# Kernel optimization log

Hardware: AMD Instinct MI355X
Metric: run time of the kernel (lower is better)

The kernel has to match this reference:

```python
import jax, jax.numpy as jnp
import numpy as np

WINDOW_SYNC = 20   # min(20, T//2) with T=8192
WINDOW_SURGE = 10
BN_EPS = 1e-5      # BatchNorm1d eval-mode, running_mean=0, running_var=1


def _corr_matrix(x):
    # x: [w, A] observations x variables -> [A, A] Pearson correlation
    xc = x - x.mean(0)
    cov = xc.T @ xc
    d = jnp.sqrt(jnp.diag(cov))
    return cov / (d[:, None] * d[None, :])


def _offdiag_mean(C):
    A = C.shape[0]
    return (C.sum() - jnp.trace(C)) / (A * (A - 1))


def _rolling_offdiag_corr(returns, window):
    # mean off-diagonal correlation over each trailing window [i-window, i)
    T, A = returns.shape
    starts = jnp.arange(T - window)
    def one(s):
        w = jax.lax.dynamic_slice(returns, (s, 0), (window, A))
        return _offdiag_mean(_corr_matrix(w))
    return jax.vmap(one)(starts)


def setup_inputs() -> dict:
    key = jax.random.key(0)
    ks = jax.random.split(key, 10)
    T, A, H = 8192, 128, 128
    returns_sequence = jax.random.normal(ks[0], (T, A), dtype=jnp.float32) * 0.02
    positions = jax.random.normal(ks[1], (A,), dtype=jnp.float32)
    s1 = 1.0 / np.sqrt(2 * A)
    s2 = 1.0 / np.sqrt(H)
    s3 = 1.0 / np.sqrt(H // 2)
    return {
        "returns_sequence": returns_sequence,
        "positions": positions,
        "w1": jax.random.uniform(ks[2], (2 * A, H), jnp.float32, -s1, s1),
        "b1": jax.random.uniform(ks[3], (H,), jnp.float32, -s1, s1),
        "gamma": jnp.ones((H,), jnp.float32),
        "beta": jnp.zeros((H,), jnp.float32),
        "w2": jax.random.uniform(ks[4], (H, H // 2), jnp.float32, -s2, s2),
        "b2": jax.random.uniform(ks[5], (H // 2,), jnp.float32, -s2, s2),
        "w3": jax.random.uniform(ks[6], (H // 2, 3), jnp.float32, -s3, s3),
        "b3": jax.random.uniform(ks[7], (3,), jnp.float32, -s3, s3),
    }


def reference(returns_sequence, positions, w1, b1, gamma, beta, w2, b2, w3, b3):
    returns = returns_sequence
    T, A = returns.shape

    # ---- herding index ----
    cs_std = jnp.std(returns, axis=1, ddof=1)                 # [T]
    herding_trend = -jnp.diff(cs_std).mean()
    avg_dispersion = cs_std.mean()
    herding_index = jnp.clip(herding_trend / (avg_dispersion + 1e-6) + 0.5, 0.0, 1.0)

    # ---- synchronization ----
    corr = _corr_matrix(returns)                              # [A, A]
    avg_correlation = _offdiag_mean(corr)
    rolling = _rolling_offdiag_corr(returns, WINDOW_SYNC)     # [T-20]
    phase_locking = (rolling > 0.7).astype(jnp.float32).mean()
    eigvals = jnp.linalg.eigvalsh(corr)
    sync_indicator = eigvals.max() / A
    sync_risk = jnp.minimum(1.0, sync_indicator * avg_correlation)

    # ---- diversity loss ----
    return_diversity = 1.0 - jnp.abs(corr).mean()             # includes diagonal (as in torch)
    pa = jnp.abs(positions)
    position_diversity = 1.0 - (pa / pa.sum()).max()
    diversity_loss = 1.0 - jnp.sqrt(return_diversity * position_diversity)

    # ---- correlation surge ----
    rolling10 = _rolling_offdiag_corr(returns, WINDOW_SURGE)  # [T-10]
    recent = rolling10[-5:].mean()
    historical = rolling10[:-5].mean()
    surge_raw = jnp.clip((recent - historical) / historical, 0.0, 1.0)
    correlation_surge = jnp.where(historical > 0, surge_raw, 0.0)

    # ---- phase coupling (pairwise sign concordance) ----
    signs = jnp.sign(returns)                                 # [T, A]
    classes = jnp.array([-1.0, 0.0, 1.0], dtype=returns.dtype)
    I = (signs[None, :, :] == classes[:, None, None]).astype(returns.dtype)  # [3, T, A]
    M = jnp.einsum('cta,ctb->ab', I, I) / T                   # eq-fraction matrix [A, A]
    avg_concordance = _offdiag_mean(M)
    phase_coupling = jnp.clip((avg_concordance - 0.5) * 2.0, 0.0, 1.0)

    # ---- herding detector MLP (BatchNorm1d in eval mode) ----
    feats = jnp.concatenate([returns[-1], positions])         # [2A]
    h = jax.nn.relu(feats @ w1 + b1)
    h = gamma * (h / jnp.sqrt(1.0 + BN_EPS)) + beta
    h = jax.nn.relu(h @ w2 + b2)
    logits = h @ w3 + b3
    herding_severity = jax.nn.softmax(logits)[2]

    collective_risk = (herding_index + sync_risk + diversity_loss) / 3.0

    return jnp.stack([herding_index, herding_severity, sync_risk, phase_locking,
                      diversity_loss, correlation_surge, phase_coupling, collective_risk])
```

## Files before the change

### kernel.cpp

```cpp
#include <hip/hip_runtime.h>
#include <math.h>

#define TN 8192
#define AN 128

#define B_GRAM 128
#define B_ROW  512
#define NW20   (TN - 20)
#define NW10   (TN - 10)
#define B_R20  2043
#define B_R10  2046
#define B_TOTAL (B_GRAM + B_ROW + B_R20 + B_R10)

#define WS_STD0    0
#define WS_STDL    1
#define WS_SUMSTD  2
#define WS_CONC    3
#define WS_SUM10   4
#define WS_SUM10L5 5
#define WS_CNT20   6
#define WS_SPEC    64
#define WS_ROWP    256
#define WS_R20V    1280
#define WS_R10V    9452
#define WS_DEND    17664

template <int W>
__device__ __forceinline__ double roll_off(const float* __restrict__ base,
                                           int lane) {
  float x0[W], x1[W];
#pragma unroll
  for (int t = 0; t < W; ++t) {
    x0[t] = base[t * AN + lane];
    x1[t] = base[t * AN + lane + 64];
  }
  float s0 = 0.f, s1 = 0.f;
#pragma unroll
  for (int t = 0; t < W; ++t) { s0 += x0[t]; s1 += x1[t]; }
  float mu0 = s0 / W, mu1 = s1 / W;
  float v0 = 0.f, v1 = 0.f;
#pragma unroll
  for (int t = 0; t < W; ++t) {
    float a = x0[t] - mu0, b = x1[t] - mu1;
    v0 += a * a;
    v1 += b * b;
  }
  float a0 = 1.0f / sqrtf(v0), a1 = 1.0f / sqrtf(v1);
  float q[W];
#pragma unroll
  for (int t = 0; t < W; ++t)
    q[t] = (x0[t] - mu0) * a0 + (x1[t] - mu1) * a1;
  int n = W;
#pragma unroll
  for (int o = 1; o <= 32; o <<= 1) {
#pragma unroll
    for (int k = 0; k < n; ++k) q[k] += __shfl_xor(q[k], o);
    if (n > 1) {
      int nh = n >> 1;
      bool hi = (lane & o) != 0;
#pragma unroll
      for (int k = 0; k < nh; ++k) q[k] = hi ? q[2 * k + 1] : q[2 * k];
      if (n & 1) { q[nh] = q[2 * nh]; n = nh + 1; } else { n = nh; }
    }
  }
  float alpha = (W == 20) ? ((lane & 16) ? 0.125f : 0.5f)
                          : ((lane & 8) ? 0.0625f : 0.25f);
  float r = q[0] * q[0] * alpha;
#pragma unroll
  for (int o = 32; o; o >>= 1) r += __shfl_xor(r, o);
  return ((double)r - (double)AN) / ((double)AN * (AN - 1));
}

__global__ void __launch_bounds__(256) k_main(const float* __restrict__ x,
                                              double* __restrict__ wsd,
                                              float* __restrict__ pc,
                                              float* __restrict__ pdg,
                                              float* __restrict__ pg) {
  int bx = blockIdx.x;
  int tid = threadIdx.x;
  if (bx < B_GRAM) {
    __shared__ float lds[8][AN];
    int i0 = (tid >> 4) * 8;
    int j0 = (tid & 15) * 8;
    int lrow = tid >> 5;
    int lcol = (tid & 31) * 4;
    const float* xs = x + (size_t)bx * 64 * AN;
    float acc[8][8];
#pragma unroll
    for (int a = 0; a < 8; ++a)
#pragma unroll
      for (int b = 0; b < 8; ++b) acc[a][b] = 0.f;
    float4 v = *(const float4*)(xs + lrow * AN + lcol);
    for (int it = 0; it < 8; ++it) {
      __syncthreads();
      *(float4*)(&lds[lrow][lcol]) = v;
      __syncthreads();
      if (it + 1 < 8)
        v = *(const float4*)(xs + ((it + 1) * 8 + lrow) * AN + lcol);
#pragma unroll
      for (int r = 0; r < 8; ++r) {
        float a[8], b[8];
        *(float4*)(a) = *(const float4*)(&lds[r][i0]);
        *(float4*)(a + 4) = *(const float4*)(&lds[r][i0 + 4]);
        *(float4*)(b) = *(const float4*)(&lds[r][j0]);
        *(float4*)(b + 4) = *(const float4*)(&lds[r][j0 + 4]);
#pragma unroll
        for (int ai = 0; ai < 8; ++ai)
#pragma unroll
          for (int bj = 0; bj < 8; ++bj)
            acc[ai][bj] = fmaf(a[ai], b[bj], acc[ai][bj]);
      }
    }
    float* dst = pg + (size_t)bx * (AN * AN);
#pragma unroll
    for (int ai = 0; ai < 8; ++ai)
#pragma unroll
      for (int bj = 0; bj < 8; bj += 4)
        *(float4*)(dst + (i0 + ai) * AN + j0 + bj) =
            make_float4(acc[ai][bj], acc[ai][bj + 1], acc[ai][bj + 2],
                        acc[ai][bj + 3]);
    if ((tid >> 4) == (tid & 15)) {
#pragma unroll
      for (int k = 0; k < 8; ++k) pdg[bx * AN + i0 + k] = acc[k][k];
    }
    if (tid < AN) {
      float cs = 0.f;
      for (int r = 0; r < 64; ++r) cs += xs[r * AN + tid];
      pc[bx * AN + tid] = cs;
    }
  } else if (bx < B_GRAM + B_ROW) {
    __shared__ double acc2[4][2];
    int rb = bx - B_GRAM;
    int lane = tid & 63;
    int w = tid >> 6;
    double sstd = 0.0, sconc = 0.0;
    for (int rr = 0; rr < 4; ++rr) {
      int t = rb * 16 + w * 4 + rr;
      const float* row = x + (size_t)t * AN;
      float x0 = row[lane], x1 = row[lane + 64];
      float s = x0 + x1;
#pragma unroll
      for (int o = 32; o; o >>= 1) s += __shfl_xor(s, o);
      float mean = s * (1.0f / AN);
      float d0 = x0 - mean, d1 = x1 - mean;
      float q = d0 * d0 + d1 * d1;
#pragma unroll
      for (int o = 32; o; o >>= 1) q += __shfl_xor(q, o);
      float sd = sqrtf(q / (float)(AN - 1));
      int pk = (int)(x0 < 0.f) + (int)(x1 < 0.f)
             + (((int)(x0 == 0.f) + (int)(x1 == 0.f)) << 10)
             + (((int)(x0 > 0.f) + (int)(x1 > 0.f)) << 20);
#pragma unroll
      for (int o = 32; o; o >>= 1) pk += __shfl_xor(pk, o);
      if (lane == 0) {
        int nn = pk & 1023, nz = (pk >> 10) & 1023, np = (pk >> 20) & 1023;
        sconc += (double)nn * nn + (double)nz * nz + (double)np * np;
        sstd += (double)sd;
        if (t == 0) wsd[WS_STD0] = (double)sd;
        if (t == TN - 1) wsd[WS_STDL] = (double)sd;
      }
    }
    if (lane == 0) { acc2[w][0] = sstd; acc2[w][1] = sconc; }
    __syncthreads();
    if (tid == 0) {
      wsd[WS_ROWP + rb * 2 + 0] = acc2[0][0] + acc2[1][0] + acc2[2][0] + acc2[3][0];
      wsd[WS_ROWP + rb * 2 + 1] = acc2[0][1] + acc2[1][1] + acc2[2][1] + acc2[3][1];
    }
  } else if (bx < B_GRAM + B_ROW + B_R20) {
    int s = (bx - (B_GRAM + B_ROW)) * 4 + (tid >> 6);
    int lane = tid & 63;
    if (s < NW20) {
      double off = roll_off<20>(x + (size_t)s * AN, lane);
      if (lane == 0) wsd[WS_R20V + s] = off;
    }
  } else {
    int s = (bx - (B_GRAM + B_ROW + B_R20)) * 4 + (tid >> 6);
    int lane = tid & 63;
    if (s < NW10) {
      double off = roll_off<10>(x + (size_t)s * AN, lane);
      if (lane == 0) wsd[WS_R10V + s] = off;
    }
  }
}

__global__ void __launch_bounds__(256) k_fold(const float* __restrict__ pc,
                                              const float* __restrict__ pdg,
                                              const float* __restrict__ pg,
                                              double* __restrict__ wsd,
                                              float* __restrict__ corr) {
  __shared__ double r0[256], r1[256], r2[256], r3[256], r4[256];
  int b = blockIdx.x;
  int t = threadIdx.x;
  if (b < 64) {
    __shared__ double muS[AN], dS[AN];
    if (t < AN) {
      double cs = 0.0, dg = 0.0;
      for (int s = 0; s < B_GRAM; ++s) {
        cs += (double)pc[s * AN + t];
        dg += (double)pdg[s * AN + t];
      }
      double mu = cs / (double)TN;
      muS[t] = mu;
      dS[t] = sqrt(dg - (double)TN * mu * mu);
    }
    __syncthreads();
    int e = b * 256 + t;
    int i = e >> 7, j = e & (AN - 1);
    double cv = 0.0;
    for (int s = 0; s < B_GRAM; ++s) cv += (double)pg[(size_t)s * (AN * AN) + e];
    cv -= (double)TN * muS[i] * muS[j];
    double c = cv / (dS[i] * dS[j]);
    corr[e] = (float)c;
    r0[t] = c;
    r1[t] = fabs(c);
    r2[t] = (i == j) ? c : 0.0;
    __syncthreads();
    for (int sft = 128; sft; sft >>= 1) {
      if (t < sft) { r0[t] += r0[t + sft]; r1[t] += r1[t + sft]; r2[t] += r2[t + sft]; }
      __syncthreads();
    }
    if (t == 0) {
      wsd[WS_SPEC + b * 3 + 0] = r0[0];
      wsd[WS_SPEC + b * 3 + 1] = r1[0];
      wsd[WS_SPEC + b * 3 + 2] = r2[0];
    }
  } else {
    double a = 0.0, bc = 0.0, cnt = 0.0, s10 = 0.0, s10l5 = 0.0;
    for (int k = t; k < 512; k += 256) {
      a += wsd[WS_ROWP + 2 * k];
      bc += wsd[WS_ROWP + 2 * k + 1];
    }
    for (int k = t; k < NW20; k += 256)
      cnt += (wsd[WS_R20V + k] > 0.7) ? 1.0 : 0.0;
    for (int k = t; k < NW10; k += 256) {
      double v = wsd[WS_R10V + k];
      s10 += v;
      if (k >= NW10 - 5) s10l5 += v;
    }
    r0[t] = a; r1[t] = bc; r2[t] = cnt; r3[t] = s10; r4[t] = s10l5;
    __syncthreads();
    for (int sft = 128; sft; sft >>= 1) {
      if (t < sft) {
        r0[t] += r0[t + sft]; r1[t] += r1[t + sft]; r2[t] += r2[t + sft];
        r3[t] += r3[t + sft]; r4[t] += r4[t + sft];
      }
      __syncthreads();
    }
    if (t == 0) {
      wsd[WS_SUMSTD] = r0[0];
      wsd[WS_CONC] = r1[0];
      wsd[WS_CNT20] = r2[0];
      wsd[WS_SUM10] = r3[0];
      wsd[WS_SUM10L5] = r4[0];
    }
  }
}

__global__ void __launch_bounds__(256) k_spec_tail(
    const float* __restrict__ x, const float* __restrict__ pos,
    const float* __restrict__ w1, const float* __restrict__ b1,
    const float* __restrict__ gamma, const float* __restrict__ beta,
    const float* __restrict__ w2, const float* __restrict__ b2,
    const float* __restrict__ w3, const float* __restrict__ b3,
    const double* __restrict__ wsd, const float* __restrict__ corr,
    float* __restrict__ out) {
  __shared__ float cS[128 * 130];
  __shared__ float vv[AN], prt[256], un[AN], red[AN];
  __shared__ double spec[3];
  __shared__ float f[2 * AN], h1[AN], h2[64], lg[3];
  int t = threadIdx.x;
  for (int e = t; e < AN * AN; e += 256)
    cS[(e >> 7) * 130 + (e & (AN - 1))] = corr[e];
  if (t < 64) {
    double s0 = wsd[WS_SPEC + t * 3 + 0];
    double s1 = wsd[WS_SPEC + t * 3 + 1];
    double s2 = wsd[WS_SPEC + t * 3 + 2];
#pragma unroll
    for (int o = 32; o; o >>= 1) {
      s0 += __shfl_xor(s0, o);
      s1 += __shfl_xor(s1, o);
      s2 += __shfl_xor(s2, o);
    }
    if (t == 0) { spec[0] = s0; spec[1] = s1; spec[2] = s2; }
  }
  f[t] = (t < AN) ? x[(size_t)(TN - 1) * AN + t] : pos[t - AN];
  if (t < AN) vv[t] = 1.0f;
  __syncthreads();
  int i = t & (AN - 1);
  int h = t >> 7;
  float lam = 0.0f;
  for (int it = 0; it < 12; ++it) {
    float acc = 0.f;
    const float* rowp = &cS[i * 130 + h * 64];
    const float* vp = &vv[h * 64];
#pragma unroll
    for (int k = 0; k < 64; k += 2) {
      float2 a = *(const float2*)(rowp + k);
      acc += a.x * vp[k] + a.y * vp[k + 1];
    }
    prt[t] = acc;
    __syncthreads();
    if (t < AN) {
      float u = prt[t] + prt[t + 128];
      un[t] = u;
      red[t] = u * u;
    }
    __syncthreads();
    for (int sft = 64; sft; sft >>= 1) {
      if (t < sft) red[t] += red[t + sft];
      __syncthreads();
    }
    lam = sqrtf(red[0]);
    if (t < AN) vv[t] = un[t] / lam;
    __syncthreads();
  }
  if (t < AN) {
    float acc = b1[t];
    for (int k = 0; k < 2 * AN; ++k) acc = fmaf(f[k], w1[k * AN + t], acc);
    acc = fmaxf(acc, 0.0f);
    acc = gamma[t] * (acc / sqrtf(1.0f + 1e-5f)) + beta[t];
    h1[t] = acc;
  }
  __syncthreads();
  if (t < 64) {
    float acc = b2[t];
    for (int k = 0; k < AN; ++k) acc = fmaf(h1[k], w2[k * 64 + t], acc);
    h2[t] = fmaxf(acc, 0.0f);
  }
  __syncthreads();
  if (t < 3) {
    float acc = b3[t];
    for (int k = 0; k < 64; ++k) acc = fmaf(h2[k], w3[k * 3 + t], acc);
    lg[t] = acc;
  }
  __syncthreads();
  if (t != 0) return;
  float m = fmaxf(lg[0], fmaxf(lg[1], lg[2]));
  float e0 = expf(lg[0] - m), e1 = expf(lg[1] - m), e2 = expf(lg[2] - m);
  double sev = (double)(e2 / (e0 + e1 + e2));
  double avg_disp = wsd[WS_SUMSTD] / (double)TN;
  double trend = -(wsd[WS_STDL] - wsd[WS_STD0]) / (double)(TN - 1);
  double hi = trend / (avg_disp + 1e-6) + 0.5;
  hi = fmin(1.0, fmax(0.0, hi));
  double avg_corr = (spec[0] - spec[2]) / ((double)AN * (AN - 1));
  double sync_ind = (double)lam / (double)AN;
  double sync_risk = fmin(1.0, sync_ind * avg_corr);
  double pl = wsd[WS_CNT20] / (double)(TN - 20);
  double rd = 1.0 - spec[1] / ((double)AN * AN);
  double pasum = 0.0, pamax = 0.0;
  for (int k = 0; k < AN; ++k) {
    double pa = fabs((double)pos[k]);
    pasum += pa;
    if (pa > pamax) pamax = pa;
  }
  double pd = 1.0 - pamax / pasum;
  double dl = 1.0 - sqrt(rd * pd);
  double recent = wsd[WS_SUM10L5] / 5.0;
  double hist = (wsd[WS_SUM10] - wsd[WS_SUM10L5]) / (double)(TN - 10 - 5);
  double sraw = (recent - hist) / hist;
  sraw = fmin(1.0, fmax(0.0, sraw));
  double surge = (hist > 0.0) ? sraw : 0.0;
  double ac = (wsd[WS_CONC] / (double)TN - (double)AN) / ((double)AN * (AN - 1));
  double pc = fmin(1.0, fmax(0.0, (ac - 0.5) * 2.0));
  double cr = (hi + sync_risk + dl) / 3.0;
  out[0] = (float)hi;
  out[1] = (float)sev;
  out[2] = (float)sync_risk;
  out[3] = (float)pl;
  out[4] = (float)dl;
  out[5] = (float)surge;
  out[6] = (float)pc;
  out[7] = (float)cr;
}

extern "C" void kernel_launch(void* const* d_in, const int* in_sizes, int n_in,
                              void* d_out, int out_size, void* d_ws, size_t ws_size,
                              hipStream_t stream) {
  const float* x     = (const float*)d_in[0];
  const float* pos   = (const float*)d_in[1];
  const float* w1    = (const float*)d_in[2];
  const float* b1    = (const float*)d_in[3];
  const float* gamma = (const float*)d_in[4];
  const float* beta  = (const float*)d_in[5];
  const float* w2    = (const float*)d_in[6];
  const float* b2    = (const float*)d_in[7];
  const float* w3    = (const float*)d_in[8];
  const float* b3    = (const float*)d_in[9];
  float* out = (float*)d_out;
  double* wsd = (double*)d_ws;
  float* corr = (float*)(wsd + WS_DEND);
  float* pc   = corr + AN * AN;
  float* pdg  = pc + B_GRAM * AN;
  float* pg   = pdg + B_GRAM * AN;

  k_main<<<B_TOTAL, 256, 0, stream>>>(x, wsd, pc, pdg, pg);
  k_fold<<<65, 256, 0, stream>>>(pc, pdg, pg, wsd, corr);
  k_spec_tail<<<1, 256, 0, stream>>>(x, pos, w1, b1, gamma, beta, w2, b2,
                                     w3, b3, wsd, corr, out);
}
```

Before: 138.0 us.

## Batch rolling windows per wave, pre-reduce per block, and trim tail kernel

Each wave now computes four consecutive rolling windows from one register strip of W+3 rows, so neighbouring windows share their loads. Because of this the rolling blocks drop from about 4000 to about 1000. The threshold count and the sums are reduced inside each block, and only per-block partials are written, so the fold kernel reads far fewer values. The tail kernel reads corr straight from global memory in the power iteration instead of staging it in LDS, and uses a wave-shuffle reduction. It also splits the first MLP layer across all 256 threads. A column-interleaved float2 load (lanes take adjacent columns) replaces the strided lane/lane+64 split, and the wave's bookkeeping stays symmetric. This adds register pressure from the larger unrolled strip.

```diff
diff --git a/kernel.cpp b/kernel.cpp
--- a/kernel.cpp
+++ b/kernel.cpp
@@ -3,72 +3,81 @@
 
 #define TN 8192
 #define AN 128
-
-#define B_GRAM 128
-#define B_ROW  512
-#define NW20   (TN - 20)
-#define NW10   (TN - 10)
-#define B_R20  2043
-#define B_R10  2046
-#define B_TOTAL (B_GRAM + B_ROW + B_R20 + B_R10)
-
-#define WS_STD0    0
-#define WS_STDL    1
-#define WS_SUMSTD  2
-#define WS_CONC    3
-#define WS_SUM10   4
-#define WS_SUM10L5 5
-#define WS_CNT20   6
-#define WS_SPEC    64
-#define WS_ROWP    256
-#define WS_R20V    1280
-#define WS_R10V    9452
-#define WS_DEND    17664
+#define NW20 (TN - 20)
+#define NW10 (TN - 10)
+
+#define NB_GRAM 128
+#define NB_ROW  512
+#define NB_R20  511
+#define NB_R10  512
+#define NB_WORK (NB_GRAM + NB_ROW + NB_R20 + NB_R10)
+
+#define WS_STD0 0
+#define WS_STDL 1
+#define WS_SPEC 8
+#define WS_BLK  200
+#define WS_DEND 4096
 
 template <int W>
-__device__ __forceinline__ double roll_off(const float* __restrict__ base,
-                                           int lane) {
-  float x0[W], x1[W];
-#pragma unroll
-  for (int t = 0; t < W; ++t) {
-    x0[t] = base[t * AN + lane];
-    x1[t] = base[t * AN + lane + 64];
-  }
-  float s0 = 0.f, s1 = 0.f;
-#pragma unroll
-  for (int t = 0; t < W; ++t) { s0 += x0[t]; s1 += x1[t]; }
-  float mu0 = s0 / W, mu1 = s1 / W;
-  float v0 = 0.f, v1 = 0.f;
-#pragma unroll
-  for (int t = 0; t < W; ++t) {
-    float a = x0[t] - mu0, b = x1[t] - mu1;
-    v0 += a * a;
-    v1 += b * b;
-  }
-  float a0 = 1.0f / sqrtf(v0), a1 = 1.0f / sqrtf(v1);
-  float q[W];
-#pragma unroll
-  for (int t = 0; t < W; ++t)
-    q[t] = (x0[t] - mu0) * a0 + (x1[t] - mu1) * a1;
-  int n = W;
-#pragma unroll
-  for (int o = 1; o <= 32; o <<= 1) {
-#pragma unroll
-    for (int k = 0; k < n; ++k) q[k] += __shfl_xor(q[k], o);
-    if (n > 1) {
-      int nh = n >> 1;
-      bool hi = (lane & o) != 0;
-#pragma unroll
-      for (int k = 0; k < nh; ++k) q[k] = hi ? q[2 * k + 1] : q[2 * k];
-      if (n & 1) { q[nh] = q[2 * nh]; n = nh + 1; } else { n = nh; }
-    }
-  }
-  float alpha = (W == 20) ? ((lane & 16) ? 0.125f : 0.5f)
-                          : ((lane & 8) ? 0.0625f : 0.25f);
-  float r = q[0] * q[0] * alpha;
-#pragma unroll
-  for (int o = 32; o; o >>= 1) r += __shfl_xor(r, o);
-  return ((double)r - (double)AN) / ((double)AN * (AN - 1));
+__device__ __forceinline__ void roll_strip4(const float* __restrict__ x,
+                                            int s0, int nwin, int lane,
+                                            double& accA, double& accB) {
+  constexpr int NR = W + 3;
+  float a0[NR], a1[NR];
+#pragma unroll
+  for (int t = 0; t < NR; ++t) {
+    int r = s0 + t; r = (r < TN) ? r : (TN - 1);
+    float2 v = *(const float2*)(x + (size_t)r * AN + 2 * lane);
+    a0[t] = v.x; a1[t] = v.y;
+  }
+#pragma unroll
+  for (int w4 = 0; w4 < 4; ++w4) {
+    int s = s0 + w4;
+    if (s < nwin) {
+      float sf0 = 0.f, sf1 = 0.f;
+#pragma unroll
+      for (int t = 0; t < W; ++t) { sf0 += a0[w4 + t]; sf1 += a1[w4 + t]; }
+      float mu0 = sf0 / W, mu1 = sf1 / W;
+      float v0 = 0.f, v1 = 0.f;
+#pragma unroll
+      for (int t = 0; t < W; ++t) {
+        float d0 = a0[w4 + t] - mu0, d1 = a1[w4 + t] - mu1;
+        v0 += d0 * d0; v1 += d1 * d1;
+      }
+      float i0 = 1.0f / sqrtf(v0), i1 = 1.0f / sqrtf(v1);
+      float q[W];
+#pragma unroll
+      for (int t = 0; t < W; ++t)
+        q[t] = (a0[w4 + t] - mu0) * i0 + (a1[w4 + t] - mu1) * i1;
+      int n = W;
+#pragma unroll
+      for (int o = 1; o <= 32; o <<= 1) {
+#pragma unroll
+        for (int k = 0; k < n; ++k) q[k] += __shfl_xor(q[k], o);
+        if (n > 1) {
+          int nh = n >> 1;
+          bool hi = (lane & o) != 0;
+#pragma unroll
+          for (int k = 0; k < nh; ++k) q[k] = hi ? q[2 * k + 1] : q[2 * k];
+          if (n & 1) { q[nh] = q[2 * nh]; n = nh + 1; } else { n = nh; }
+        }
+      }
+      float alpha = (W == 20) ? ((lane & 16) ? 0.125f : 0.5f)
+                              : ((lane & 8) ? 0.0625f : 0.25f);
+      float r = q[0] * q[0] * alpha;
+#pragma unroll
+      for (int o = 32; o; o >>= 1) r += __shfl_xor(r, o);
+      if (lane == 0) {
+        double off = ((double)r - (double)AN) / ((double)AN * (AN - 1));
+        if (W == 20) {
+          accA += (off > 0.7) ? 1.0 : 0.0;
+        } else {
+          accA += off;
+          if (s >= TN - W - 5) accB += off;
+        }
+      }
+    }
+  }
 }
 
 __global__ void __launch_bounds__(256) k_main(const float* __restrict__ x,
@@ -76,42 +85,48 @@
                                               float* __restrict__ pc,
                                               float* __restrict__ pdg,
                                               float* __restrict__ pg) {
-  int bx = blockIdx.x;
-  int tid = threadIdx.x;
-  if (bx < B_GRAM) {
-    __shared__ float lds[8][AN];
+  __shared__ union {
+    float stage[8][AN];
+    double tacc[4][2];
+  } sm;
+  const int b = blockIdx.x;
+  const int tid = threadIdx.x;
+  const int lane = tid & 63;
+  const int w = tid >> 6;
+
+  if (b < NB_GRAM) {
     int i0 = (tid >> 4) * 8;
     int j0 = (tid & 15) * 8;
     int lrow = tid >> 5;
     int lcol = (tid & 31) * 4;
-    const float* xs = x + (size_t)bx * 64 * AN;
+    const float* xs = x + (size_t)b * 64 * AN;
     float acc[8][8];
 #pragma unroll
     for (int a = 0; a < 8; ++a)
 #pragma unroll
-      for (int b = 0; b < 8; ++b) acc[a][b] = 0.f;
+      for (int c = 0; c < 8; ++c) acc[a][c] = 0.f;
     float4 v = *(const float4*)(xs + lrow * AN + lcol);
     for (int it = 0; it < 8; ++it) {
       __syncthreads();
-      *(float4*)(&lds[lrow][lcol]) = v;
+      *(float4*)(&sm.stage[lrow][lcol]) = v;
       __syncthreads();
       if (it + 1 < 8)
         v = *(const float4*)(xs + ((it + 1) * 8 + lrow) * AN + lcol);
 #pragma unroll
       for (int r = 0; r < 8; ++r) {
-        float a[8], b[8];
-        *(float4*)(a) = *(const float4*)(&lds[r][i0]);
-        *(float4*)(a + 4) = *(const float4*)(&lds[r][i0 + 4]);
-        *(float4*)(b) = *(const float4*)(&lds[r][j0]);
-        *(float4*)(b + 4) = *(const float4*)(&lds[r][j0 + 4]);
+        float aa[8], bb[8];
+        *(float4*)(aa) = *(const float4*)(&sm.stage[r][i0]);
+        *(float4*)(aa + 4) = *(const float4*)(&sm.stage[r][i0 + 4]);
+        *(float4*)(bb) = *(const float4*)(&sm.stage[r][j0]);
+        *(float4*)(bb + 4) = *(const float4*)(&sm.stage[r][j0 + 4]);
 #pragma unroll
         for (int ai = 0; ai < 8; ++ai)
 #pragma unroll
           for (int bj = 0; bj < 8; ++bj)
-            acc[ai][bj] = fmaf(a[ai], b[bj], acc[ai][bj]);
-      }
-    }
-    float* dst = pg + (size_t)bx * (AN * AN);
+            acc[ai][bj] = fmaf(aa[ai], bb[bj], acc[ai][bj]);
+      }
+    }
+    float* dst = pg + (size_t)b * (AN * AN);
 #pragma unroll
     for (int ai = 0; ai < 8; ++ai)
 #pragma unroll
@@ -121,23 +136,23 @@
                         acc[ai][bj + 3]);
     if ((tid >> 4) == (tid & 15)) {
 #pragma unroll
-      for (int k = 0; k < 8; ++k) pdg[bx * AN + i0 + k] = acc[k][k];
+      for (int k = 0; k < 8; ++k) pdg[b * AN + i0 + k] = acc[k][k];
     }
     if (tid < AN) {
       float cs = 0.f;
       for (int r = 0; r < 64; ++r) cs += xs[r * AN + tid];
-      pc[bx * AN + tid] = cs;
-    }
-  } else if (bx < B_GRAM + B_ROW) {
-    __shared__ double acc2[4][2];
-    int rb = bx - B_GRAM;
-    int lane = tid & 63;
-    int w = tid >> 6;
+      pc[b * AN + tid] = cs;
+    }
+    return;
+  }
+
+  if (b < NB_GRAM + NB_ROW) {
+    int rb = b - NB_GRAM;
     double sstd = 0.0, sconc = 0.0;
     for (int rr = 0; rr < 4; ++rr) {
       int t = rb * 16 + w * 4 + rr;
-      const float* row = x + (size_t)t * AN;
-      float x0 = row[lane], x1 = row[lane + 64];
+      float2 xv = *(const float2*)(x + (size_t)t * AN + 2 * lane);
+      float x0 = xv.x, x1 = xv.y;
       float s = x0 + x1;
 #pragma unroll
       for (int o = 32; o; o >>= 1) s += __shfl_xor(s, o);
@@ -160,25 +175,40 @@
         if (t == TN - 1) wsd[WS_STDL] = (double)sd;
       }
     }
-    if (lane == 0) { acc2[w][0] = sstd; acc2[w][1] = sconc; }
+    if (lane == 0) { sm.tacc[w][0] = sstd; sm.tacc[w][1] = sconc; }
     __syncthreads();
     if (tid == 0) {
-      wsd[WS_ROWP + rb * 2 + 0] = acc2[0][0] + acc2[1][0] + acc2[2][0] + acc2[3][0];
-      wsd[WS_ROWP + rb * 2 + 1] = acc2[0][1] + acc2[1][1] + acc2[2][1] + acc2[3][1];
-    }
-  } else if (bx < B_GRAM + B_ROW + B_R20) {
-    int s = (bx - (B_GRAM + B_ROW)) * 4 + (tid >> 6);
-    int lane = tid & 63;
-    if (s < NW20) {
-      double off = roll_off<20>(x + (size_t)s * AN, lane);
-      if (lane == 0) wsd[WS_R20V + s] = off;
-    }
-  } else {
-    int s = (bx - (B_GRAM + B_ROW + B_R20)) * 4 + (tid >> 6);
-    int lane = tid & 63;
-    if (s < NW10) {
-      double off = roll_off<10>(x + (size_t)s * AN, lane);
-      if (lane == 0) wsd[WS_R10V + s] = off;
+      wsd[WS_BLK + (size_t)b * 2 + 0] =
+          sm.tacc[0][0] + sm.tacc[1][0] + sm.tacc[2][0] + sm.tacc[3][0];
+      wsd[WS_BLK + (size_t)b * 2 + 1] =
+          sm.tacc[0][1] + sm.tacc[1][1] + sm.tacc[2][1] + sm.tacc[3][1];
+    }
+    return;
+  }
+
+  if (b < NB_GRAM + NB_ROW + NB_R20) {
+    int s0 = (b - (NB_GRAM + NB_ROW)) * 16 + w * 4;
+    double cnt = 0.0, dummy = 0.0;
+    roll_strip4<20>(x, s0, NW20, lane, cnt, dummy);
+    if (lane == 0) { sm.tacc[w][0] = cnt; }
+    __syncthreads();
+    if (tid == 0)
+      wsd[WS_BLK + (size_t)b * 2 + 0] =
+          sm.tacc[0][0] + sm.tacc[1][0] + sm.tacc[2][0] + sm.tacc[3][0];
+    return;
+  }
+
+  {
+    int s0 = (b - (NB_GRAM + NB_ROW + NB_R20)) * 16 + w * 4;
+    double s10 = 0.0, s10l5 = 0.0;
+    roll_strip4<10>(x, s0, NW10, lane, s10, s10l5);
+    if (lane == 0) { sm.tacc[w][0] = s10; sm.tacc[w][1] = s10l5; }
+    __syncthreads();
+    if (tid == 0) {
+      wsd[WS_BLK + (size_t)b * 2 + 0] =
+          sm.tacc[0][0] + sm.tacc[1][0] + sm.tacc[2][0] + sm.tacc[3][0];
+      wsd[WS_BLK + (size_t)b * 2 + 1] =
+          sm.tacc[0][1] + sm.tacc[1][1] + sm.tacc[2][1] + sm.tacc[3][1];
     }
   }
 }
@@ -195,7 +225,7 @@
     __shared__ double muS[AN], dS[AN];
     if (t < AN) {
       double cs = 0.0, dg = 0.0;
-      for (int s = 0; s < B_GRAM; ++s) {
+      for (int s = 0; s < NB_GRAM; ++s) {
         cs += (double)pc[s * AN + t];
         dg += (double)pdg[s * AN + t];
       }
@@ -207,7 +237,7 @@
     int e = b * 256 + t;
     int i = e >> 7, j = e & (AN - 1);
     double cv = 0.0;
-    for (int s = 0; s < B_GRAM; ++s) cv += (double)pg[(size_t)s * (AN * AN) + e];
+    for (int s = 0; s < NB_GRAM; ++s) cv += (double)pg[(size_t)s * (AN * AN) + e];
     cv -= (double)TN * muS[i] * muS[j];
     double c = cv / (dS[i] * dS[j]);
     corr[e] = (float)c;
@@ -226,16 +256,11 @@
     }
   } else {
     double a = 0.0, bc = 0.0, cnt = 0.0, s10 = 0.0, s10l5 = 0.0;
-    for (int k = t; k < 512; k += 256) {
-      a += wsd[WS_ROWP + 2 * k];
-      bc += wsd[WS_ROWP + 2 * k + 1];
-    }
-    for (int k = t; k < NW20; k += 256)
-      cnt += (wsd[WS_R20V + k] > 0.7) ? 1.0 : 0.0;
-    for (int k = t; k < NW10; k += 256) {
-      double v = wsd[WS_R10V + k];
-      s10 += v;
-      if (k >= NW10 - 5) s10l5 += v;
+    for (int k = NB_GRAM + t; k < NB_WORK; k += 256) {
+      const double* p = wsd + WS_BLK + (size_t)k * 2;
+      if (k < NB_GRAM + NB_ROW) { a += p[0]; bc += p[1]; }
+      else if (k < NB_GRAM + NB_ROW + NB_R20) cnt += p[0];
+      else { s10 += p[0]; s10l5 += p[1]; }
     }
     r0[t] = a; r1[t] = bc; r2[t] = cnt; r3[t] = s10; r4[t] = s10l5;
     __syncthreads();
@@ -247,11 +272,11 @@
       __syncthreads();
     }
     if (t == 0) {
-      wsd[WS_SUMSTD] = r0[0];
-      wsd[WS_CONC] = r1[0];
-      wsd[WS_CNT20] = r2[0];
-      wsd[WS_SUM10] = r3[0];
-      wsd[WS_SUM10L5] = r4[0];
+      wsd[2] = r0[0];
+      wsd[3] = r1[0];
+      wsd[4] = r2[0];
+      wsd[5] = r3[0];
+      wsd[6] = r4[0];
     }
   }
 }
@@ -264,13 +289,12 @@
     const float* __restrict__ w3, const float* __restrict__ b3,
     const double* __restrict__ wsd, const float* __restrict__ corr,
     float* __restrict__ out) {
-  __shared__ float cS[128 * 130];
-  __shared__ float vv[AN], prt[256], un[AN], red[AN];
+  __shared__ float vv[AN], prt[256], un[AN], red[4];
   __shared__ double spec[3];
   __shared__ float f[2 * AN], h1[AN], h2[64], lg[3];
   int t = threadIdx.x;
-  for (int e = t; e < AN * AN; e += 256)
-    cS[(e >> 7) * 130 + (e & (AN - 1))] = corr[e];
+  int lane = t & 63;
+  int w = t >> 6;
   if (t < 64) {
     double s0 = wsd[WS_SPEC + t * 3 + 0];
     double s1 = wsd[WS_SPEC + t * 3 + 1];
@@ -286,40 +310,45 @@
   f[t] = (t < AN) ? x[(size_t)(TN - 1) * AN + t] : pos[t - AN];
   if (t < AN) vv[t] = 1.0f;
   __syncthreads();
-  int i = t & (AN - 1);
-  int h = t >> 7;
+  int ri = t & (AN - 1), hh = t >> 7;
+  const float4* rp = (const float4*)(corr + ri * AN + hh * 64);
   float lam = 0.0f;
   for (int it = 0; it < 12; ++it) {
+    const float4* vp = (const float4*)(&vv[hh * 64]);
     float acc = 0.f;
-    const float* rowp = &cS[i * 130 + h * 64];
-    const float* vp = &vv[h * 64];
-#pragma unroll
-    for (int k = 0; k < 64; k += 2) {
-      float2 a = *(const float2*)(rowp + k);
-      acc += a.x * vp[k] + a.y * vp[k + 1];
+#pragma unroll
+    for (int k = 0; k < 16; ++k) {
+      float4 a = rp[k], bv = vp[k];
+      acc += a.x * bv.x + a.y * bv.y + a.z * bv.z + a.w * bv.w;
     }
     prt[t] = acc;
     __syncthreads();
     if (t < AN) {
       float u = prt[t] + prt[t + 128];
       un[t] = u;
-      red[t] = u * u;
-    }
-    __syncthreads();
-    for (int sft = 64; sft; sft >>= 1) {
-      if (t < sft) red[t] += red[t + sft];
-      __syncthreads();
-    }
-    lam = sqrtf(red[0]);
+      float sq = u * u;
+#pragma unroll
+      for (int o = 32; o; o >>= 1) sq += __shfl_xor(sq, o);
+      if (lane == 0) red[w] = sq;
+    }
+    __syncthreads();
+    lam = sqrtf(red[0] + red[1]);
     if (t < AN) vv[t] = un[t] / lam;
     __syncthreads();
   }
+  {
+    int n = t & 127, h = t >> 7;
+    float acc = 0.f;
+    const float* wcol = w1 + h * 128 * AN + n;
+    const float* fv = f + h * 128;
+    for (int k = 0; k < 128; ++k) acc = fmaf(fv[k], wcol[k * AN], acc);
+    prt[t] = acc;
+  }
+  __syncthreads();
   if (t < AN) {
-    float acc = b1[t];
-    for (int k = 0; k < 2 * AN; ++k) acc = fmaf(f[k], w1[k * AN + t], acc);
+    float acc = b1[t] + prt[t] + prt[t + 128];
     acc = fmaxf(acc, 0.0f);
-    acc = gamma[t] * (acc / sqrtf(1.0f + 1e-5f)) + beta[t];
-    h1[t] = acc;
+    h1[t] = gamma[t] * (acc / sqrtf(1.0f + 1e-5f)) + beta[t];
   }
   __syncthreads();
   if (t < 64) {
@@ -338,14 +367,16 @@
   float m = fmaxf(lg[0], fmaxf(lg[1], lg[2]));
   float e0 = expf(lg[0] - m), e1 = expf(lg[1] - m), e2 = expf(lg[2] - m);
   double sev = (double)(e2 / (e0 + e1 + e2));
-  double avg_disp = wsd[WS_SUMSTD] / (double)TN;
+  double sumstd = wsd[2], conc = wsd[3], cnt20 = wsd[4];
+  double sum10 = wsd[5], sum10l5 = wsd[6];
+  double avg_disp = sumstd / (double)TN;
   double trend = -(wsd[WS_STDL] - wsd[WS_STD0]) / (double)(TN - 1);
   double hi = trend / (avg_disp + 1e-6) + 0.5;
   hi = fmin(1.0, fmax(0.0, hi));
   double avg_corr = (spec[0] - spec[2]) / ((double)AN * (AN - 1));
   double sync_ind = (double)lam / (double)AN;
   double sync_risk = fmin(1.0, sync_ind * avg_corr);
-  double pl = wsd[WS_CNT20] / (double)(TN - 20);
+  double pl = cnt20 / (double)(TN - 20);
   double rd = 1.0 - spec[1] / ((double)AN * AN);
   double pasum = 0.0, pamax = 0.0;
   for (int k = 0; k < AN; ++k) {
@@ -355,13 +386,13 @@
   }
   double pd = 1.0 - pamax / pasum;
   double dl = 1.0 - sqrt(rd * pd);
-  double recent = wsd[WS_SUM10L5] / 5.0;
-  double hist = (wsd[WS_SUM10] - wsd[WS_SUM10L5]) / (double)(TN - 10 - 5);
+  double recent = sum10l5 / 5.0;
+  double hist = (sum10 - sum10l5) / (double)(TN - 10 - 5);
   double sraw = (recent - hist) / hist;
   sraw = fmin(1.0, fmax(0.0, sraw));
   double surge = (hist > 0.0) ? sraw : 0.0;
-  double ac = (wsd[WS_CONC] / (double)TN - (double)AN) / ((double)AN * (AN - 1));
-  double pc = fmin(1.0, fmax(0.0, (ac - 0.5) * 2.0));
+  double ac = (conc / (double)TN - (double)AN) / ((double)AN * (AN - 1));
+  double pcup = fmin(1.0, fmax(0.0, (ac - 0.5) * 2.0));
   double cr = (hi + sync_risk + dl) / 3.0;
   out[0] = (float)hi;
   out[1] = (float)sev;
@@ -369,7 +400,7 @@
   out[3] = (float)pl;
   out[4] = (float)dl;
   out[5] = (float)surge;
-  out[6] = (float)pc;
+  out[6] = (float)pcup;
   out[7] = (float)cr;
 }
 
@@ -390,10 +421,10 @@
   double* wsd = (double*)d_ws;
   float* corr = (float*)(wsd + WS_DEND);
   float* pc   = corr + AN * AN;
-  float* pdg  = pc + B_GRAM * AN;
-  float* pg   = pdg + B_GRAM * AN;
-
-  k_main<<<B_TOTAL, 256, 0, stream>>>(x, wsd, pc, pdg, pg);
+  float* pdg  = pc + NB_GRAM * AN;
+  float* pg   = pdg + NB_GRAM * AN;
+
+  k_main<<<NB_WORK, 256, 0, stream>>>(x, wsd, pc, pdg, pg);
   k_fold<<<65, 256, 0, stream>>>(pc, pdg, pg, wsd, corr);
   k_spec_tail<<<1, 256, 0, stream>>>(x, pos, w1, b1, gamma, beta, w2, b2,
                                      w3, b3, wsd, corr, out);
```

After: 125.6 us. -9.0%, faster.
